# Optimization experiments

Measured on AMD Instinct MI355X. Metric: run time of the kernel, lower is better.

The kernel has to match this reference:

```python
import jax, jax.numpy as jnp
import numpy as np

N = 50000
IN_C = 128
OUT_C = 64


def gcn_conv(x, edge_index, W, b):
    # PyG GCNConv: h = X W; add self-loops; symmetric norm D^-1/2 (A+I) D^-1/2; aggregate; + bias
    n = x.shape[0]
    h = x @ W  # [N, out]
    loop = jnp.arange(n, dtype=edge_index.dtype)
    row = jnp.concatenate([edge_index[0], loop])  # source
    col = jnp.concatenate([edge_index[1], loop])  # target
    deg = jax.ops.segment_sum(jnp.ones_like(col, dtype=h.dtype), col, num_segments=n)
    dinv = jnp.where(deg > 0, jax.lax.rsqrt(deg), 0.0)
    norm = dinv[row] * dinv[col]  # [E+N]
    msg = norm[:, None] * h[row]  # gather source features
    out = jax.ops.segment_sum(msg, col, num_segments=n)  # scatter to targets
    return out + b


def layer_norm(x, w, b, eps=1e-5):
    mu = jnp.mean(x, axis=-1, keepdims=True)
    var = jnp.mean((x - mu) ** 2, axis=-1, keepdims=True)
    return (x - mu) * jax.lax.rsqrt(var + eps) * w + b


def setup_inputs() -> dict:
    key = jax.random.key(0)
    ks = jax.random.split(key, 10)
    x = jax.random.normal(ks[0], (N, IN_C), dtype=jnp.float32)
    edge_index = jax.random.randint(ks[1], (2, 800000), 0, N, dtype=jnp.int64)
    s1 = 1.0 / np.sqrt(IN_C)
    s2 = 1.0 / np.sqrt(OUT_C)
    W1 = jax.random.uniform(ks[2], (IN_C, OUT_C), jnp.float32, -s1, s1)
    b1 = jnp.zeros((OUT_C,), jnp.float32)
    ln_w = jnp.ones((OUT_C,), jnp.float32)
    ln_b = jnp.zeros((OUT_C,), jnp.float32)
    W2 = jax.random.uniform(ks[3], (OUT_C, OUT_C), jnp.float32, -s2, s2)
    b2 = jnp.zeros((OUT_C,), jnp.float32)
    W3 = jax.random.uniform(ks[4], (OUT_C, 6), jnp.float32, -s2, s2)
    b3 = jax.random.uniform(ks[5], (6,), jnp.float32, -s2, s2)
    return {"x": x, "edge_index": edge_index, "W1": W1, "b1": b1,
            "ln_w": ln_w, "ln_b": ln_b, "W2": W2, "b2": b2, "W3": W3, "b3": b3}


def reference(x, edge_index, W1, b1, ln_w, ln_b, W2, b2, W3, b3):
    h = gcn_conv(x, edge_index, W1, b1)           # [N, 64]
    h = jax.nn.relu(layer_norm(h, ln_w, ln_b))    # [N, 64]
    out1 = gcn_conv(h, edge_index, W2, b2)        # [N, 64]
    out2 = jax.nn.sigmoid(h @ W3 + b3)            # [N, 6]
    return (out1, out2)
```

## Files before the change

### kernel.cpp

```cpp
#include <hip/hip_runtime.h>
#include <hip/hip_fp16.h>
#include <math.h>


#define ELLW 48

typedef _Float16 half8 __attribute__((ext_vector_type(8)));
typedef float f32x4 __attribute__((ext_vector_type(4)));

__global__ void k_init(int* __restrict__ cnt, int n) {
    int i = blockIdx.x * blockDim.x + threadIdx.x;
    if (i < n) cnt[i] = 0;
}

__global__ void k_scatter(const int* __restrict__ row, const int* __restrict__ col,
                          int* __restrict__ cnt, int* __restrict__ ell, int E) {
    int e = blockIdx.x * blockDim.x + threadIdx.x;
    if (e < E) {
        int c = col[e];
        int r = atomicAdd(&cnt[c], 1);
        if (r < ELLW) ell[c * ELLW + r] = row[e] << 7;
    }
}

__global__ void k_dinv(const int* __restrict__ cnt, float* __restrict__ dinv, int n) {
    int i = blockIdx.x * blockDim.x + threadIdx.x;
    if (i < n) dinv[i] = rsqrtf((float)(cnt[i] + 1));
}

__global__ void k_pack(const float* __restrict__ W1, const float* __restrict__ W2,
                       const float* __restrict__ W3, _Float16* __restrict__ W1g,
                       _Float16* __restrict__ Bg) {
    int idx = blockIdx.x * 256 + threadIdx.x;
    if (idx < 8192) {
        int j = idx & 7, L = (idx >> 3) & 63, s = (idx >> 9) & 3, t = idx >> 11;
        int k = s * 32 + (L >> 4) * 8 + j;
        int c = t * 16 + (L & 15);
        W1g[idx] = (_Float16)W1[k * 64 + c];
    } else if (idx < 8192 + 5120) {
        int i2 = idx - 8192;
        int j = i2 & 7, L = (i2 >> 3) & 63, s = (i2 >> 9) & 1, u = i2 >> 10;
        int k = s * 32 + (L >> 4) * 8 + j;
        int c = (L & 15);
        float v;
        if (u < 4) v = W2[k * 64 + u * 16 + c];
        else v = (c < 6) ? W3[k * 6 + c] : 0.f;
        Bg[i2] = (_Float16)v;
    }
}

__global__ __launch_bounds__(256, 4) void k_gemm1(
    const float* __restrict__ x, const _Float16* __restrict__ W1g,
    const float* __restrict__ dinv, uint* __restrict__ hs,
    uint* __restrict__ h2s, int n) {
    int tid = threadIdx.x;
    if (blockIdx.x == 0) {
        if (tid < 32) hs[(size_t)n * 32 + tid] = 0u;
        else if (tid < 64) h2s[(size_t)n * 32 + (tid - 32)] = 0u;
    }
    int lane = tid & 63, wid = tid >> 6;
    int m16 = lane & 15, quad = lane >> 4;
    int node0 = blockIdx.x * 64 + wid * 16;
    int arow = node0 + m16;
    if (arow >= n) arow = n - 1;
    const float* xr = x + (size_t)arow * 128;
    half8 A[4];
#pragma unroll
    for (int s = 0; s < 4; s++) {
        const float4* p = (const float4*)(xr + s * 32 + quad * 8);
        float4 f0 = p[0], f1 = p[1];
        half8 a;
        a[0] = (_Float16)f0.x; a[1] = (_Float16)f0.y;
        a[2] = (_Float16)f0.z; a[3] = (_Float16)f0.w;
        a[4] = (_Float16)f1.x; a[5] = (_Float16)f1.y;
        a[6] = (_Float16)f1.z; a[7] = (_Float16)f1.w;
        A[s] = a;
    }
    float dsc[4];
#pragma unroll
    for (int r = 0; r < 4; r++) {
        int nd = node0 + quad * 4 + r;
        dsc[r] = dinv[nd < n ? nd : n - 1];
    }
    const half8* Wv = (const half8*)W1g;
#pragma unroll
    for (int t = 0; t < 4; t++) {
        f32x4 acc = {0.f, 0.f, 0.f, 0.f};
#pragma unroll
        for (int s = 0; s < 4; s++)
            acc = __builtin_amdgcn_mfma_f32_16x16x32_f16(A[s], Wv[(t * 4 + s) * 64 + lane], acc, 0, 0, 0);
#pragma unroll
        for (int r = 0; r < 4; r++) {
            int nd = node0 + quad * 4 + r;
            float v = acc[r] * dsc[r];
            float vo = __shfl_xor(v, 1, 64);
            if (!(m16 & 1) && nd < n) {
                __half2 pk = __floats2half2_rn(v, vo);
                hs[(size_t)nd * 32 + t * 8 + (m16 >> 1)] = *(uint*)&pk;
            }
        }
    }
}

#define GATHER_BODY(SRC)                                                      \
    int4 o1[4], o2[4];                                                        \
    uint4 u0[4], u1[4];                                                       \
    {                                                                         \
        int4 o0[4];                                                           \
        _Pragma("unroll") for (int p = 0; p < 4; p++) o0[p] = ldidx(p, 0);    \
        _Pragma("unroll") for (int p = 0; p < 4; p++) o1[p] = ldidx(p, 8);    \
        _Pragma("unroll") for (int p = 0; p < 4; p++) {                       \
            u0[p].x = *(const uint*)(SRC + o0[p].x + m4);                     \
            u0[p].y = *(const uint*)(SRC + o0[p].y + m4);                     \
            u0[p].z = *(const uint*)(SRC + o0[p].z + m4);                     \
            u0[p].w = *(const uint*)(SRC + o0[p].w + m4);                     \
        }                                                                     \
    }                                                                         \
    for (int jb = 0; jb < Pmax; jb += 8) {                                    \
        _Pragma("unroll") for (int p = 0; p < 4; p++) o2[p] = ldidx(p, jb + 16); \
        _Pragma("unroll") for (int p = 0; p < 4; p++) {                       \
            u1[p].x = *(const uint*)(SRC + o1[p].x + m4);                     \
            u1[p].y = *(const uint*)(SRC + o1[p].y + m4);                     \
            u1[p].z = *(const uint*)(SRC + o1[p].z + m4);                     \
            u1[p].w = *(const uint*)(SRC + o1[p].w + m4);                     \
        }                                                                     \
        _Pragma("unroll") for (int p = 0; p < 4; p++) {                       \
            float2 f;                                                         \
            f = __half22float2(*(__half2*)&u0[p].x); ax[p] += f.x; ay[p] += f.y; \
            f = __half22float2(*(__half2*)&u0[p].y); ax[p] += f.x; ay[p] += f.y; \
            f = __half22float2(*(__half2*)&u0[p].z); ax[p] += f.x; ay[p] += f.y; \
            f = __half22float2(*(__half2*)&u0[p].w); ax[p] += f.x; ay[p] += f.y; \
        }                                                                     \
        _Pragma("unroll") for (int p = 0; p < 4; p++) { o1[p] = o2[p]; u0[p] = u1[p]; } \
    }

__global__ __launch_bounds__(256, 4) void k_conv1_fused(
    const uint* __restrict__ hs, const int* __restrict__ ell,
    const int* __restrict__ cnt, const float* __restrict__ dinv,
    const float* __restrict__ b1, const float* __restrict__ lnw_g,
    const float* __restrict__ lnb_g, const _Float16* __restrict__ Bg,
    const float* __restrict__ b3, uint* __restrict__ h2s,
    float* __restrict__ out2, int zoff, int n) {
    __shared__ _Float16 Y[4][16 * 72];
    int tid = threadIdx.x;
    int lane = tid & 63, wid = tid >> 6;
    int m = lane & 31, g = lane >> 5;
    int m4 = m * 4;
    {
        float4 z = {0.f, 0.f, 0.f, 0.f};
        float4* yb = (float4*)Y[wid];
        for (int i = lane; i < 144; i += 64) yb[i] = z;
    }
    int base = blockIdx.x * 16;
    int nid[4], st[4], P[4];
    int Pmax = 0;
#pragma unroll
    for (int p = 0; p < 4; p++) {
        int node = base + wid * 4 + p;
        if (node >= n) node = n - 1;
        nid[p] = node;
        st[p] = node * ELLW;
        P[p] = cnt[node];
        Pmax = Pmax > P[p] ? Pmax : P[p];
    }
    Pmax = (Pmax + 7) & ~7;
    auto ldidx = [&](int p, int jb) -> int4 {
        int4 o = *(const int4*)(ell + st[p] + jb + 4 * g);
        int b = jb + 4 * g;
        o.x = (b + 0 < P[p]) ? o.x : zoff;
        o.y = (b + 1 < P[p]) ? o.y : zoff;
        o.z = (b + 2 < P[p]) ? o.z : zoff;
        o.w = (b + 3 < P[p]) ? o.w : zoff;
        return o;
    };
    const char* hsb = (const char*)hs;
    float ax[4], ay[4];
#pragma unroll
    for (int p = 0; p < 4; p++) {
        int sa = (g == 0) ? (nid[p] << 7) : zoff;
        uint us = *(const uint*)(hsb + sa + m4);
        float2 f = __half22float2(*(__half2*)&us);
        ax[p] = f.x; ay[p] = f.y;
    }
    GATHER_BODY(hsb)

    float2 b1v = ((const float2*)b1)[m];
    float2 lw = ((const float2*)lnw_g)[m];
    float2 lb = ((const float2*)lnb_g)[m];
    float dcs[4];
#pragma unroll
    for (int p = 0; p < 4; p++) {
        float axp = ax[p] + __shfl_xor(ax[p], 32, 64);
        float ayp = ay[p] + __shfl_xor(ay[p], 32, 64);
        float dc = dinv[nid[p]];
        dcs[p] = dc;
        float va = fmaf(dc, axp, b1v.x);
        float vb = fmaf(dc, ayp, b1v.y);
        float s = va + vb;
#pragma unroll
        for (int off = 16; off > 0; off >>= 1) s += __shfl_xor(s, off, 64);
        float mu = s * (1.f / 64.f);
        float da = va - mu, db = vb - mu;
        float q = da * da + db * db;
#pragma unroll
        for (int off = 16; off > 0; off >>= 1) q += __shfl_xor(q, off, 64);
        float rstd = rsqrtf(q * (1.f / 64.f) + 1e-5f);
        float yA = fmaxf(fmaf(da * rstd, lw.x, lb.x), 0.f);
        float yB = fmaxf(fmaf(db * rstd, lw.y, lb.y), 0.f);
        if (g == 0) {
            __half2 pk = __floats2half2_rn(yA, yB);
            *(__half2*)&Y[wid][p * 72 + 2 * m] = pk;
        }
    }
    int m16 = lane & 15, quad = lane >> 4;
    half8 a0 = *(const half8*)&Y[wid][m16 * 72 + quad * 8];
    half8 a1 = *(const half8*)&Y[wid][m16 * 72 + 32 + quad * 8];
    const half8* Bv = (const half8*)Bg;
    _Float16* h2h = (_Float16*)h2s;
#pragma unroll
    for (int t = 0; t < 4; t++) {
        f32x4 acc = {0.f, 0.f, 0.f, 0.f};
        acc = __builtin_amdgcn_mfma_f32_16x16x32_f16(a0, Bv[(t * 2 + 0) * 64 + lane], acc, 0, 0, 0);
        acc = __builtin_amdgcn_mfma_f32_16x16x32_f16(a1, Bv[(t * 2 + 1) * 64 + lane], acc, 0, 0, 0);
#pragma unroll
        for (int r = 0; r < 4; r++) {
            int nodep = base + wid * 4 + r;
            if (quad == 0 && nodep < n)
                h2h[(size_t)nodep * 64 + t * 16 + m16] = (_Float16)(acc[r] * dcs[r]);
        }
    }
    {
        f32x4 acc = {0.f, 0.f, 0.f, 0.f};
        acc = __builtin_amdgcn_mfma_f32_16x16x32_f16(a0, Bv[8 * 64 + lane], acc, 0, 0, 0);
        acc = __builtin_amdgcn_mfma_f32_16x16x32_f16(a1, Bv[9 * 64 + lane], acc, 0, 0, 0);
        float bb = b3[m16 < 6 ? m16 : 0];
#pragma unroll
        for (int r = 0; r < 4; r++) {
            int nodep = base + wid * 4 + r;
            if (quad == 0 && m16 < 6 && nodep < n)
                out2[(size_t)nodep * 6 + m16] = 1.f / (1.f + __expf(-(acc[r] + bb)));
        }
    }
}

__global__ __launch_bounds__(256, 4) void k_conv2(
    const uint* __restrict__ h2s, const int* __restrict__ ell,
    const int* __restrict__ cnt, const float* __restrict__ dinv,
    const float* __restrict__ b2, float* __restrict__ out1, int zoff, int n) {
    int tid = threadIdx.x;
    int lane = tid & 63, wid = tid >> 6;
    int m = lane & 31, g = lane >> 5;
    int m4 = m * 4;
    int base = blockIdx.x * 16;
    int nid[4], st[4], P[4];
    int Pmax = 0;
#pragma unroll
    for (int p = 0; p < 4; p++) {
        int node = base + wid * 4 + p;
        if (node >= n) node = n - 1;
        nid[p] = node;
        st[p] = node * ELLW;
        P[p] = cnt[node];
        Pmax = Pmax > P[p] ? Pmax : P[p];
    }
    Pmax = (Pmax + 7) & ~7;
    auto ldidx = [&](int p, int jb) -> int4 {
        int4 o = *(const int4*)(ell + st[p] + jb + 4 * g);
        int b = jb + 4 * g;
        o.x = (b + 0 < P[p]) ? o.x : zoff;
        o.y = (b + 1 < P[p]) ? o.y : zoff;
        o.z = (b + 2 < P[p]) ? o.z : zoff;
        o.w = (b + 3 < P[p]) ? o.w : zoff;
        return o;
    };
    const char* hsb = (const char*)h2s;
    float ax[4], ay[4];
#pragma unroll
    for (int p = 0; p < 4; p++) {
        int sa = (g == 0) ? (nid[p] << 7) : zoff;
        uint us = *(const uint*)(hsb + sa + m4);
        float2 f = __half22float2(*(__half2*)&us);
        ax[p] = f.x; ay[p] = f.y;
    }
    GATHER_BODY(hsb)

    float2 b2v = ((const float2*)b2)[m];
#pragma unroll
    for (int p = 0; p < 4; p++) {
        float axp = ax[p] + __shfl_xor(ax[p], 32, 64);
        float ayp = ay[p] + __shfl_xor(ay[p], 32, 64);
        int node = base + wid * 4 + p;
        if (g == 0 && node < n) {
            float dc = dinv[nid[p]];
            float2 r;
            r.x = fmaf(dc, axp, b2v.x);
            r.y = fmaf(dc, ayp, b2v.y);
            ((float2*)out1)[(size_t)node * 32 + m] = r;
        }
    }
}

extern "C" void kernel_launch(void* const* d_in, const int* in_sizes, int n_in,
                              void* d_out, int out_size, void* d_ws, size_t ws_size,
                              hipStream_t stream) {
    const float* x   = (const float*)d_in[0];
    const int*   ei  = (const int*)d_in[1];
    const float* W1  = (const float*)d_in[2];
    const float* b1  = (const float*)d_in[3];
    const float* lnw = (const float*)d_in[4];
    const float* lnb = (const float*)d_in[5];
    const float* W2  = (const float*)d_in[6];
    const float* b2  = (const float*)d_in[7];
    const float* W3  = (const float*)d_in[8];
    const float* b3  = (const float*)d_in[9];

    int n = in_sizes[0] / 128;
    int E = in_sizes[1] / 2;
    const int* row = ei;
    const int* col = ei + E;

    char* ws = (char*)d_ws;
    size_t off = 0;
    auto carve = [&](size_t bytes) -> char* {
        char* p = ws + off;
        off = (off + bytes + 255) & ~(size_t)255;
        return p;
    };
    int*   cnt  = (int*)carve(4 * (size_t)n);
    float* dinv = (float*)carve(4 * (size_t)n);
    int*   ell  = (int*)carve(4 * ((size_t)n * ELLW + 256));
    uint*  hs   = (uint*)carve(128 * ((size_t)n + 1));
    uint*  h2s  = (uint*)carve(128 * ((size_t)n + 1));
    _Float16* W1g = (_Float16*)carve(2 * 8192);
    _Float16* Bg  = (_Float16*)carve(2 * 5120);

    float* out1 = (float*)d_out;
    float* out2 = out1 + (size_t)n * 64;
    int zero_off = n << 7;

    k_pack<<<52, 256, 0, stream>>>(W1, W2, W3, W1g, Bg);
    k_init<<<(n + 255) / 256, 256, 0, stream>>>(cnt, n);
    k_scatter<<<(E + 255) / 256, 256, 0, stream>>>(row, col, cnt, ell, E);
    k_dinv<<<(n + 255) / 256, 256, 0, stream>>>(cnt, dinv, n);
    k_gemm1<<<(n + 63) / 64, 256, 0, stream>>>(x, W1g, dinv, hs, h2s, n);
    k_conv1_fused<<<(n + 15) / 16, 256, 0, stream>>>(hs, ell, cnt, dinv,
                                                     b1, lnw, lnb, Bg, b3,
                                                     h2s, out2, zero_off, n);
    k_conv2<<<(n + 15) / 16, 256, 0, stream>>>(h2s, ell, cnt, dinv, b2,
                                               out1, zero_off, n);
}
```

Before: 210.2 us.

## Partition ELL scatter by destination slice across XCD-mapped blocks

The edge scatter kernel now splits destination nodes into 8 slices keyed on blockIdx&7, so each block handles only atomics whose target falls in its slice. Every slice group reads all edges with int4 vector loads in a grid-stride loop. The aim is to keep each node's counter atomics and ELL writes inside one XCD's L2, which lines up with the round-robin block-to-XCD dispatch on MI355X, and to reduce cross-die atomic traffic. In exchange the edge arrays are read 8 times, and it relies on the row and col pointers being 16-byte aligned.

```diff
diff --git a/kernel.cpp b/kernel.cpp
--- a/kernel.cpp
+++ b/kernel.cpp
@@ -13,13 +13,46 @@
     if (i < n) cnt[i] = 0;
 }
 
-__global__ void k_scatter(const int* __restrict__ row, const int* __restrict__ col,
-                          int* __restrict__ cnt, int* __restrict__ ell, int E) {
-    int e = blockIdx.x * blockDim.x + threadIdx.x;
-    if (e < E) {
-        int c = col[e];
-        int r = atomicAdd(&cnt[c], 1);
-        if (r < ELLW) ell[c * ELLW + r] = row[e] << 7;
+__global__ __launch_bounds__(256) void k_scatter(
+    const int* __restrict__ row, const int* __restrict__ col,
+    int* __restrict__ cnt, int* __restrict__ ell, int E, int slice_sz) {
+    int slice = blockIdx.x & 7;
+    int lo = slice * slice_sz;
+    int hi = lo + slice_sz;
+    int nchunk = gridDim.x >> 3;
+    int stride = nchunk * 256;
+    int v0 = (blockIdx.x >> 3) * 256 + threadIdx.x;
+    int nv = E >> 2;
+    const int4* c4p = (const int4*)col;
+    const int4* r4p = (const int4*)row;
+    for (int v = v0; v < nv; v += stride) {
+        int4 c4 = c4p[v];
+        int4 r4 = r4p[v];
+        if (c4.x >= lo && c4.x < hi) {
+            int rk = atomicAdd(&cnt[c4.x], 1);
+            if (rk < ELLW) ell[c4.x * ELLW + rk] = r4.x << 7;
+        }
+        if (c4.y >= lo && c4.y < hi) {
+            int rk = atomicAdd(&cnt[c4.y], 1);
+            if (rk < ELLW) ell[c4.y * ELLW + rk] = r4.y << 7;
+        }
+        if (c4.z >= lo && c4.z < hi) {
+            int rk = atomicAdd(&cnt[c4.z], 1);
+            if (rk < ELLW) ell[c4.z * ELLW + rk] = r4.z << 7;
+        }
+        if (c4.w >= lo && c4.w < hi) {
+            int rk = atomicAdd(&cnt[c4.w], 1);
+            if (rk < ELLW) ell[c4.w * ELLW + rk] = r4.w << 7;
+        }
+    }
+    if ((blockIdx.x >> 3) == 0) {
+        for (int e = (nv << 2) + threadIdx.x; e < E; e += 256) {
+            int c = col[e];
+            if (c >= lo && c < hi) {
+                int rk = atomicAdd(&cnt[c], 1);
+                if (rk < ELLW) ell[c * ELLW + rk] = row[e] << 7;
+            }
+        }
     }
 }
 
@@ -337,10 +370,11 @@
     float* out1 = (float*)d_out;
     float* out2 = out1 + (size_t)n * 64;
     int zero_off = n << 7;
+    int slice_sz = (n + 7) / 8;
 
     k_pack<<<52, 256, 0, stream>>>(W1, W2, W3, W1g, Bg);
     k_init<<<(n + 255) / 256, 256, 0, stream>>>(cnt, n);
-    k_scatter<<<(E + 255) / 256, 256, 0, stream>>>(row, col, cnt, ell, E);
+    k_scatter<<<8 * 256, 256, 0, stream>>>(row, col, cnt, ell, E, slice_sz);
     k_dinv<<<(n + 255) / 256, 256, 0, stream>>>(cnt, dinv, n);
     k_gemm1<<<(n + 63) / 64, 256, 0, stream>>>(x, W1g, dinv, hs, h2s, n);
     k_conv1_fused<<<(n + 15) / 16, 256, 0, stream>>>(hs, ell, cnt, dinv,
```

Measured after the change: 202.5 us. 1.04x faster.
